# Kernel tuning notes

Hardware: AMD Instinct MI355X
Metric: run time of the kernel (lower is better)

## Reference

```python
import jax, jax.numpy as jnp
import numpy as np

BS, NF, N, J, NOUT = 8, 64, 2048, 3, 64
EPS = 1e-5


def setup_inputs() -> dict:
    key = jax.random.key(0)
    ks = jax.random.split(key, 6)
    X = jax.random.normal(ks[0], (BS, NF, N), dtype=jnp.float32)
    W = jax.random.normal(ks[1], (BS, N, N, J), dtype=jnp.float32)
    N_batch = jnp.ones((BS,), jnp.float32) * N  # valid nodes per graph
    mask = jnp.ones((BS, 1, N), jnp.float32)
    scale = 0.1  # matches _init_weights
    cv1_w = scale * jax.random.normal(ks[2], (NOUT, J * NF), jnp.float32)
    cv1_b = scale * jax.random.normal(ks[3], (NOUT,), jnp.float32)
    cv2_w = scale * jax.random.normal(ks[4], (NOUT, J * NF), jnp.float32)
    cv2_b = scale * jax.random.normal(ks[5], (NOUT,), jnp.float32)
    bn_gamma = jnp.ones((2 * NOUT,), jnp.float32)
    bn_beta = jnp.zeros((2 * NOUT,), jnp.float32)
    return {"X": X, "W": W, "N_batch": N_batch, "mask": mask,
            "cv1_w": cv1_w, "cv1_b": cv1_b, "cv2_w": cv2_w, "cv2_b": cv2_b,
            "bn_gamma": bn_gamma, "bn_beta": bn_beta}


def reference(X, W, N_batch, mask, cv1_w, cv1_b, cv2_w, cv2_b, bn_gamma, bn_beta):
    bs, nf, n = X.shape
    j = W.shape[3]
    # graph_oper: out[b, j*nf:(j+1)*nf, m] = (A[b,:,:,j] @ X[b].T).T
    #           = sum_n W[b,m,n,j] * X[b,f,n]  -> fused batched contraction
    x1 = jnp.einsum('bmnj,bfn->bjfm', W, X).reshape(bs, j * nf, n)
    # conv1x1 (kernel size 1) == per-node matmul over channels
    y1 = jnp.einsum('oi,bin->bon', cv1_w, x1) + cv1_b[None, :, None]
    z1 = jax.nn.relu(y1)
    yl1 = jax.nn.relu(jnp.einsum('oi,bin->bon', cv2_w, x1) + cv2_b[None, :, None])
    zb = jnp.concatenate([yl1, z1], axis=1)  # (bs, 2*NOUT, N)
    # masked graph batch-norm: per-channel stats over all valid nodes in the batch
    total = jnp.sum(N_batch)
    mean = jnp.sum(zb * mask, axis=(0, 2)) / total
    cz = zb - mean[None, :, None]
    var = jnp.sum(mask * cz * cz, axis=(0, 2)) / total
    zbn = cz * jax.lax.rsqrt(var + EPS)[None, :, None]
    zbn = (bn_gamma[None, :, None] * zbn + bn_beta[None, :, None]) * mask
    return (zbn, W)
```

## Files before the change

### kernel.cpp

```cpp
#include <hip/hip_runtime.h>
#include <hip/hip_bf16.h>


#define EPSV 1e-5f
#define ZBN_ELEMS (8*128*2048)

typedef __bf16 bf16x8 __attribute__((ext_vector_type(8)));
typedef float  f32x4  __attribute__((ext_vector_type(4)));
typedef float  f4v    __attribute__((ext_vector_type(4)));

union BF8 { unsigned short u[8]; bf16x8 v; };

__device__ __forceinline__ unsigned short f2bf(float f) {
    unsigned u = __float_as_uint(f);
    u += 0x7fffu + ((u >> 16) & 1u);
    return (unsigned short)(u >> 16);
}

__global__ void prep_kernel(const float* __restrict__ X,
                            unsigned short* __restrict__ Xbf,
                            float* __restrict__ stats) {
    int t = blockIdx.x * 256 + threadIdx.x;
    Xbf[t] = f2bf(X[t]);
    if (blockIdx.x == 0 && threadIdx.x < 256) stats[threadIdx.x] = 0.0f;
}

__global__ __launch_bounds__(256, 4) void gemm_conv_kernel(
    const float* __restrict__ W,
    const unsigned short* __restrict__ Xbf,
    const float* __restrict__ cv1_w, const float* __restrict__ cv1_b,
    const float* __restrict__ cv2_w, const float* __restrict__ cv2_b,
    float* __restrict__ out, float* __restrict__ stats)
{
    __shared__ float red[2][16][196];
    __shared__ unsigned short x1s[16][200];

    const int tid  = threadIdx.x;
    const int w    = tid >> 6;
    const int lane = tid & 63;
    const int q    = lane >> 4;
    const int l15  = lane & 15;
    const int bx   = blockIdx.x;
    const int b    = bx >> 7;
    const int mt   = bx & 127;

    const int m_global = mt * 16 + l15;
    const float* Wrow = W   + (size_t)(b * 2048 + m_global) * 6144;
    float*       Wout = out + (size_t)ZBN_ELEMS + (size_t)(b * 2048 + m_global) * 6144;
    const unsigned short* Xb = Xbf + b * (64 * 2048);
    const int kbase = w * 512;

    f32x4 acc[4][3];
    #pragma unroll
    for (int ft = 0; ft < 4; ++ft)
        #pragma unroll
        for (int j = 0; j < 3; ++j)
            acc[ft][j] = (f32x4)0.0f;

    #pragma unroll 2
    for (int kt = 0; kt < 16; ++kt) {
        const int n0 = kbase + kt * 32 + q * 8;
        const f4v* wp = (const f4v*)(Wrow + n0 * 3);
        f4v wv[6];
        #pragma unroll
        for (int i = 0; i < 6; ++i) wv[i] = __builtin_nontemporal_load(wp + i);
        f4v* wo = (f4v*)(Wout + n0 * 3);
        #pragma unroll
        for (int i = 0; i < 6; ++i) wo[i] = wv[i];

        const float* wf = (const float*)wv;
        BF8 a[3];
        #pragma unroll
        for (int j = 0; j < 3; ++j)
            #pragma unroll
            for (int e = 0; e < 8; ++e)
                a[j].u[e] = f2bf(wf[e * 3 + j]);

        BF8 bfr[4];
        #pragma unroll
        for (int ft = 0; ft < 4; ++ft)
            bfr[ft].v = *(const bf16x8*)(Xb + (ft * 16 + l15) * 2048 + n0);

        #pragma unroll
        for (int ft = 0; ft < 4; ++ft)
            #pragma unroll
            for (int j = 0; j < 3; ++j)
                acc[ft][j] = __builtin_amdgcn_mfma_f32_16x16x32_bf16(a[j].v, bfr[ft].v, acc[ft][j], 0, 0, 0);
    }

    if (w >= 2) {
        float* buf = (float*)red[w - 2];
        #pragma unroll
        for (int ft = 0; ft < 4; ++ft)
            #pragma unroll
            for (int j = 0; j < 3; ++j)
                #pragma unroll
                for (int r = 0; r < 4; ++r)
                    buf[(q * 4 + r) * 196 + j * 64 + ft * 16 + l15] = acc[ft][j][r];
    }
    __syncthreads();
    if (w < 2) {
        const float* buf = (const float*)red[w];
        #pragma unroll
        for (int ft = 0; ft < 4; ++ft)
            #pragma unroll
            for (int j = 0; j < 3; ++j)
                #pragma unroll
                for (int r = 0; r < 4; ++r)
                    acc[ft][j][r] += buf[(q * 4 + r) * 196 + j * 64 + ft * 16 + l15];
    }
    __syncthreads();
    if (w == 1) {
        float* buf = (float*)red[0];
        #pragma unroll
        for (int ft = 0; ft < 4; ++ft)
            #pragma unroll
            for (int j = 0; j < 3; ++j)
                #pragma unroll
                for (int r = 0; r < 4; ++r)
                    buf[(q * 4 + r) * 196 + j * 64 + ft * 16 + l15] = acc[ft][j][r];
    }
    __syncthreads();
    if (w == 0) {
        const float* buf = (const float*)red[0];
        #pragma unroll
        for (int ft = 0; ft < 4; ++ft)
            #pragma unroll
            for (int j = 0; j < 3; ++j)
                #pragma unroll
                for (int r = 0; r < 4; ++r) {
                    float v = acc[ft][j][r] + buf[(q * 4 + r) * 196 + j * 64 + ft * 16 + l15];
                    x1s[q * 4 + r][j * 64 + ft * 16 + l15] = f2bf(v);
                }
    }
    __syncthreads();

    f32x4 acc2[2];
    acc2[0] = (f32x4)0.0f;
    acc2[1] = (f32x4)0.0f;

    #pragma unroll
    for (int kt = 0; kt < 6; ++kt) {
        const int i0 = kt * 32 + q * 8;
        BF8 afr[2];
        #pragma unroll
        for (int ctl = 0; ctl < 2; ++ctl) {
            const int c = (2 * w + ctl) * 16 + l15;
            const float* wr = (c < 64) ? (cv2_w + c * 192) : (cv1_w + (c - 64) * 192);
            const f4v* wp2 = (const f4v*)(wr + i0);
            f4v w0 = wp2[0], w1 = wp2[1];
            #pragma unroll
            for (int e = 0; e < 4; ++e) {
                afr[ctl].u[e]     = f2bf(w0[e]);
                afr[ctl].u[e + 4] = f2bf(w1[e]);
            }
        }
        BF8 b2;
        b2.v = *(const bf16x8*)(&x1s[l15][i0]);
        #pragma unroll
        for (int ctl = 0; ctl < 2; ++ctl)
            acc2[ctl] = __builtin_amdgcn_mfma_f32_16x16x32_bf16(afr[ctl].v, b2.v, acc2[ctl], 0, 0, 0);
    }

    #pragma unroll
    for (int ctl = 0; ctl < 2; ++ctl) {
        #pragma unroll
        for (int r = 0; r < 4; ++r) {
            const int c = (2 * w + ctl) * 16 + q * 4 + r;
            const float bias = (c < 64) ? cv2_b[c] : cv1_b[c - 64];
            float zv = acc2[ctl][r] + bias;
            zv = fmaxf(zv, 0.0f);
            out[((size_t)(b * 128 + c) << 11) + mt * 16 + l15] = zv;
            float s1 = zv, s2 = zv * zv;
            #pragma unroll
            for (int msk = 1; msk < 16; msk <<= 1) {
                s1 += __shfl_xor(s1, msk);
                s2 += __shfl_xor(s2, msk);
            }
            if (l15 == 0) {
                atomicAdd(&stats[c], s1);
                atomicAdd(&stats[128 + c], s2);
            }
        }
    }
}

__global__ void finalize_kernel(const float* __restrict__ stats,
                                const float* __restrict__ Nb,
                                const float* __restrict__ gamma,
                                const float* __restrict__ beta,
                                float* __restrict__ ss) {
    int c = threadIdx.x;
    float total = 0.0f;
    #pragma unroll
    for (int i = 0; i < 8; ++i) total += Nb[i];
    float mean = stats[c] / total;
    float var  = stats[128 + c] / total - mean * mean;
    float inv  = rsqrtf(var + EPSV);
    float sc   = gamma[c] * inv;
    ss[c]       = sc;
    ss[128 + c] = beta[c] - mean * sc;
}

__global__ void norm_kernel(float* __restrict__ out,
                            const float* __restrict__ ss,
                            const float* __restrict__ mask) {
    int t = blockIdx.x * 256 + threadIdx.x;
    float4 v = ((const float4*)out)[t];
    int row = t >> 9;
    int c = row & 127;
    int b = row >> 7;
    float sc = ss[c], sh = ss[128 + c];
    float4 mk = ((const float4*)mask)[(b << 9) + (t & 511)];
    float4 r;
    r.x = (v.x * sc + sh) * mk.x;
    r.y = (v.y * sc + sh) * mk.y;
    r.z = (v.z * sc + sh) * mk.z;
    r.w = (v.w * sc + sh) * mk.w;
    ((float4*)out)[t] = r;
}

extern "C" void kernel_launch(void* const* d_in, const int* in_sizes, int n_in,
                              void* d_out, int out_size, void* d_ws, size_t ws_size,
                              hipStream_t stream) {
    const float* X     = (const float*)d_in[0];
    const float* W     = (const float*)d_in[1];
    const float* Nb    = (const float*)d_in[2];
    const float* mask  = (const float*)d_in[3];
    const float* cv1_w = (const float*)d_in[4];
    const float* cv1_b = (const float*)d_in[5];
    const float* cv2_w = (const float*)d_in[6];
    const float* cv2_b = (const float*)d_in[7];
    const float* gamma = (const float*)d_in[8];
    const float* beta  = (const float*)d_in[9];
    float* out = (float*)d_out;

    unsigned short* Xbf = (unsigned short*)d_ws;
    float* stats = (float*)((char*)d_ws + (size_t)2 * 1024 * 1024);
    float* ss    = stats + 256;

    hipLaunchKernelGGL(prep_kernel,      dim3(4096), dim3(256), 0, stream, X, Xbf, stats);
    hipLaunchKernelGGL(gemm_conv_kernel, dim3(1024), dim3(256), 0, stream,
                       W, Xbf, cv1_w, cv1_b, cv2_w, cv2_b, out, stats);
    hipLaunchKernelGGL(finalize_kernel,  dim3(1),    dim3(128), 0, stream, stats, Nb, gamma, beta, ss);
    hipLaunchKernelGGL(norm_kernel,      dim3(2048), dim3(256), 0, stream, out, ss, mask);
}
```

Before: 881.5 us.

## Stage W tiles through LDS with coalesced loads and split features across waves

The main GEMM loop now loads W with fully coalesced row-contiguous loads across the whole block. It transposes each 16x128x3 tile into LDS as bf16, and each wave handles 16 of the 64 features over the full K range, replacing the per-lane strided row reads and the cross-wave K-split reduction. W loads are double-buffered in registers to overlap the next tile's fetch with the current MFMA work. This adds two barriers per tile and scattered 2-byte LDS writes, which may cause bank conflicts.

```diff
diff --git a/kernel.cpp b/kernel.cpp
--- a/kernel.cpp
+++ b/kernel.cpp
@@ -10,6 +10,7 @@
 typedef float  f4v    __attribute__((ext_vector_type(4)));
 
 union BF8 { unsigned short u[8]; bf16x8 v; };
+union F4  { float f[4]; f4v v; };
 
 __device__ __forceinline__ unsigned short f2bf(float f) {
     unsigned u = __float_as_uint(f);
@@ -32,7 +33,7 @@
     const float* __restrict__ cv2_w, const float* __restrict__ cv2_b,
     float* __restrict__ out, float* __restrict__ stats)
 {
-    __shared__ float red[2][16][196];
+    __shared__ unsigned short wt[3][16][136];
     __shared__ unsigned short x1s[16][200];
 
     const int tid  = threadIdx.x;
@@ -40,99 +41,82 @@
     const int lane = tid & 63;
     const int q    = lane >> 4;
     const int l15  = lane & 15;
-    const int bx   = blockIdx.x;
-    const int b    = bx >> 7;
-    const int mt   = bx & 127;
-
-    const int m_global = mt * 16 + l15;
-    const float* Wrow = W   + (size_t)(b * 2048 + m_global) * 6144;
-    float*       Wout = out + (size_t)ZBN_ELEMS + (size_t)(b * 2048 + m_global) * 6144;
-    const unsigned short* Xb = Xbf + b * (64 * 2048);
-    const int kbase = w * 512;
-
-    f32x4 acc[4][3];
-    #pragma unroll
-    for (int ft = 0; ft < 4; ++ft)
-        #pragma unroll
-        for (int j = 0; j < 3; ++j)
-            acc[ft][j] = (f32x4)0.0f;
-
-    #pragma unroll 2
-    for (int kt = 0; kt < 16; ++kt) {
-        const int n0 = kbase + kt * 32 + q * 8;
-        const f4v* wp = (const f4v*)(Wrow + n0 * 3);
-        f4v wv[6];
-        #pragma unroll
-        for (int i = 0; i < 6; ++i) wv[i] = __builtin_nontemporal_load(wp + i);
-        f4v* wo = (f4v*)(Wout + n0 * 3);
-        #pragma unroll
-        for (int i = 0; i < 6; ++i) wo[i] = wv[i];
-
-        const float* wf = (const float*)wv;
-        BF8 a[3];
-        #pragma unroll
-        for (int j = 0; j < 3; ++j)
-            #pragma unroll
-            for (int e = 0; e < 8; ++e)
-                a[j].u[e] = f2bf(wf[e * 3 + j]);
-
+    const int b    = blockIdx.x >> 7;
+    const int mt   = blockIdx.x & 127;
+
+    const float* Wbase  = W   + (size_t)(b * 2048 + mt * 16) * 6144;
+    float*       Wobase = out + (size_t)ZBN_ELEMS + (size_t)(b * 2048 + mt * 16) * 6144;
+    const unsigned short* Xrow = Xbf + (size_t)b * (64 * 2048) + (w * 16 + l15) * 2048;
+
+    int gofs[6];
+    int crow[6], co4[6];
+    #pragma unroll
+    for (int i = 0; i < 6; ++i) {
+        int c  = tid + 256 * i;
+        int r  = c / 96;
+        int o4 = (c - r * 96) * 4;
+        crow[i] = r; co4[i] = o4;
+        gofs[i] = r * 6144 + o4;
+    }
+
+    f32x4 acc[3];
+    acc[0] = (f32x4)0.0f; acc[1] = (f32x4)0.0f; acc[2] = (f32x4)0.0f;
+
+    auto process = [&](F4 (&buf)[6], int t) {
+        #pragma unroll
+        for (int i = 0; i < 6; ++i)
+            *(f4v*)(Wobase + t * 384 + gofs[i]) = buf[i].v;
+        #pragma unroll
+        for (int i = 0; i < 6; ++i) {
+            #pragma unroll
+            for (int u = 0; u < 4; ++u) {
+                int o = co4[i] + u;
+                int n = o / 3;
+                int j = o - n * 3;
+                ((unsigned short*)wt)[(j * 16 + crow[i]) * 136 + n] = f2bf(buf[i].f[u]);
+            }
+        }
+        __syncthreads();
         BF8 bfr[4];
         #pragma unroll
-        for (int ft = 0; ft < 4; ++ft)
-            bfr[ft].v = *(const bf16x8*)(Xb + (ft * 16 + l15) * 2048 + n0);
-
-        #pragma unroll
-        for (int ft = 0; ft < 4; ++ft)
-            #pragma unroll
-            for (int j = 0; j < 3; ++j)
-                acc[ft][j] = __builtin_amdgcn_mfma_f32_16x16x32_bf16(a[j].v, bfr[ft].v, acc[ft][j], 0, 0, 0);
-    }
-
-    if (w >= 2) {
-        float* buf = (float*)red[w - 2];
-        #pragma unroll
-        for (int ft = 0; ft < 4; ++ft)
-            #pragma unroll
-            for (int j = 0; j < 3; ++j)
-                #pragma unroll
-                for (int r = 0; r < 4; ++r)
-                    buf[(q * 4 + r) * 196 + j * 64 + ft * 16 + l15] = acc[ft][j][r];
-    }
-    __syncthreads();
-    if (w < 2) {
-        const float* buf = (const float*)red[w];
-        #pragma unroll
-        for (int ft = 0; ft < 4; ++ft)
-            #pragma unroll
-            for (int j = 0; j < 3; ++j)
-                #pragma unroll
-                for (int r = 0; r < 4; ++r)
-                    acc[ft][j][r] += buf[(q * 4 + r) * 196 + j * 64 + ft * 16 + l15];
-    }
-    __syncthreads();
-    if (w == 1) {
-        float* buf = (float*)red[0];
-        #pragma unroll
-        for (int ft = 0; ft < 4; ++ft)
-            #pragma unroll
-            for (int j = 0; j < 3; ++j)
-                #pragma unroll
-                for (int r = 0; r < 4; ++r)
-                    buf[(q * 4 + r) * 196 + j * 64 + ft * 16 + l15] = acc[ft][j][r];
-    }
-    __syncthreads();
-    if (w == 0) {
-        const float* buf = (const float*)red[0];
-        #pragma unroll
-        for (int ft = 0; ft < 4; ++ft)
-            #pragma unroll
-            for (int j = 0; j < 3; ++j)
-                #pragma unroll
-                for (int r = 0; r < 4; ++r) {
-                    float v = acc[ft][j][r] + buf[(q * 4 + r) * 196 + j * 64 + ft * 16 + l15];
-                    x1s[q * 4 + r][j * 64 + ft * 16 + l15] = f2bf(v);
-                }
-    }
+        for (int kk = 0; kk < 4; ++kk)
+            bfr[kk].v = *(const bf16x8*)(Xrow + t * 128 + kk * 32 + q * 8);
+        #pragma unroll
+        for (int kk = 0; kk < 4; ++kk) {
+            #pragma unroll
+            for (int j = 0; j < 3; ++j) {
+                bf16x8 af = *(const bf16x8*)&wt[j][l15][kk * 32 + q * 8];
+                acc[j] = __builtin_amdgcn_mfma_f32_16x16x32_bf16(af, bfr[kk].v, acc[j], 0, 0, 0);
+            }
+        }
+        __syncthreads();
+    };
+
+    F4 bufA[6], bufB[6];
+    #pragma unroll
+    for (int i = 0; i < 6; ++i)
+        bufA[i].v = __builtin_nontemporal_load((const f4v*)(Wbase + gofs[i]));
+
+    #pragma unroll 1
+    for (int tt = 0; tt < 8; ++tt) {
+        const int t0 = 2 * tt, t1 = 2 * tt + 1;
+        #pragma unroll
+        for (int i = 0; i < 6; ++i)
+            bufB[i].v = __builtin_nontemporal_load((const f4v*)(Wbase + t1 * 384 + gofs[i]));
+        process(bufA, t0);
+        if (tt < 7) {
+            #pragma unroll
+            for (int i = 0; i < 6; ++i)
+                bufA[i].v = __builtin_nontemporal_load((const f4v*)(Wbase + (t1 + 1) * 384 + gofs[i]));
+        }
+        process(bufB, t1);
+    }
+
+    #pragma unroll
+    for (int j = 0; j < 3; ++j)
+        #pragma unroll
+        for (int r = 0; r < 4; ++r)
+            x1s[q * 4 + r][j * 64 + w * 16 + l15] = f2bf(acc[j][r]);
     __syncthreads();
 
     f32x4 acc2[2];
```

After: 771.5 us. 12.5% less time.
